# Kernel tuning notes

Measured on AMD Instinct MI355X. Metric: run time of the kernel, lower is better.

Reference implementation:

```python
import jax, jax.numpy as jnp
import numpy as np

N = 20000      # tuple-graph nodes
E = 320000     # edges per relation
F_IN = 5189    # 80 one-hot + 3*1703 node features
DIM = 256
N_ORIG = 183   # original texas graph nodes
C = 7


def _gcn(x, W, b, src, dst, n):
    # PyG GCNConv: add self loops, symmetric deg^-1/2 normalization, aggregate src->dst.
    loop = jnp.arange(n)
    s = jnp.concatenate([src, loop])
    d = jnp.concatenate([dst, loop])
    deg = jax.ops.segment_sum(jnp.ones(s.shape[0], x.dtype), d, num_segments=n)
    dinv = jnp.where(deg > 0, jax.lax.rsqrt(deg), 0.0)
    norm = dinv[s] * dinv[d]            # [E+n]
    h = x @ W                            # [n, dim]
    out = jax.ops.segment_sum(h[s] * norm[:, None], d, num_segments=n)
    return out + b


def _mlp(h, w1, b1, w2, b2):
    return jnp.maximum(h @ w1 + b1, 0.0) @ w2 + b2


def _seg_mean(h, idx, n):
    s = jax.ops.segment_sum(h, idx, num_segments=n)
    cnt = jax.ops.segment_sum(jnp.ones(idx.shape[0], h.dtype), idx, num_segments=n)
    return s / jnp.maximum(cnt, 1.0)[:, None]


def setup_inputs() -> dict:
    key = jax.random.key(0)
    ks = jax.random.split(key, 16)
    sc_in = 1.0 / np.sqrt(F_IN)
    sc_d = 1.0 / np.sqrt(DIM)
    sc_3d = 1.0 / np.sqrt(3 * DIM)
    inp = {
        'x': jax.random.normal(ks[0], (N, F_IN), jnp.float32),
        'w1': jax.random.normal(ks[1], (3, F_IN, DIM), jnp.float32) * sc_in,
        'b1': jnp.zeros((3, DIM), jnp.float32),
        'w2': jax.random.normal(ks[2], (3, DIM, DIM), jnp.float32) * sc_d,
        'b2': jnp.zeros((3, DIM), jnp.float32),
        'm1w1': jax.random.normal(ks[3], (3 * DIM, DIM), jnp.float32) * sc_3d,
        'm1b1': jnp.zeros((DIM,), jnp.float32),
        'm1w2': jax.random.normal(ks[4], (DIM, DIM), jnp.float32) * sc_d,
        'm1b2': jnp.zeros((DIM,), jnp.float32),
        'm2w1': jax.random.normal(ks[5], (3 * DIM, DIM), jnp.float32) * sc_3d,
        'm2b1': jnp.zeros((DIM,), jnp.float32),
        'm2w2': jax.random.normal(ks[6], (DIM, DIM), jnp.float32) * sc_d,
        'm2b2': jnp.zeros((DIM,), jnp.float32),
        'mw1': jax.random.normal(ks[7], (3 * DIM, DIM), jnp.float32) * sc_3d,
        'mb1': jnp.zeros((DIM,), jnp.float32),
        'mw2': jax.random.normal(ks[8], (DIM, C), jnp.float32) * sc_d,
        'mb2': jnp.zeros((C,), jnp.float32),
        'edge_index_1': jax.random.randint(ks[9], (2, E), 0, N),
        'edge_index_2': jax.random.randint(ks[10], (2, E), 0, N),
        'edge_index_3': jax.random.randint(ks[11], (2, E), 0, N),
        'index_1': jax.random.randint(ks[12], (N,), 0, N_ORIG),
        'index_2': jax.random.randint(ks[13], (N,), 0, N_ORIG),
        'index_3': jax.random.randint(ks[14], (N,), 0, N_ORIG),
    }
    return inp


def reference(x, w1, b1, w2, b2, m1w1, m1b1, m1w2, m1b2,
              m2w1, m2b1, m2w2, m2b2, mw1, mb1, mw2, mb2,
              edge_index_1, edge_index_2, edge_index_3,
              index_1, index_2, index_3):
    n = x.shape[0]
    eis = (edge_index_1, edge_index_2, edge_index_3)
    # layer 1: three GCN convs over the three relations, ReLU, concat, MLP
    hs = [jnp.maximum(_gcn(x, w1[i], b1[i], eis[i][0], eis[i][1], n), 0.0) for i in range(3)]
    h = _mlp(jnp.concatenate(hs, axis=-1), m1w1, m1b1, m1w2, m1b2)
    # layer 2
    hs = [jnp.maximum(_gcn(h, w2[i], b2[i], eis[i][0], eis[i][1], n), 0.0) for i in range(3)]
    h = _mlp(jnp.concatenate(hs, axis=-1), m2w1, m2b1, m2w2, m2b2)
    # faithful to source bug: index_2 is overwritten by index_3 before scatter
    x1 = _seg_mean(h, index_1, N_ORIG)
    x2 = _seg_mean(h, index_3, N_ORIG)
    x3 = _seg_mean(h, index_3, N_ORIG)
    out = _mlp(jnp.concatenate([x1, x2, x3], axis=1), mw1, mb1, mw2, mb2)
    return jax.nn.log_softmax(out, axis=1)
```

## Files before the change

kernel.cpp:

```cpp
#include <hip/hip_runtime.h>
#include <hip/hip_bf16.h>
#include <cstdint>
#include <cstddef>

typedef __bf16 bf16_t;
typedef __bf16 bf16x8 __attribute__((ext_vector_type(8)));
typedef __bf16 bf16x4 __attribute__((ext_vector_type(4)));
typedef float f32x4 __attribute__((ext_vector_type(4)));

#define NN 20000
#define NE 320000
#define FIN 5189
#define KP1 5216
#define NORIG 183

__device__ inline f32x4 ld4u(const float* p) {
  f32x4 v; __builtin_memcpy(&v, p, 16); return v;
}

__device__ inline void gload_lds16(const bf16_t* g, bf16_t* l) {
  __builtin_amdgcn_global_load_lds(
      (const __attribute__((address_space(1))) uint32_t*)g,
      (__attribute__((address_space(3))) uint32_t*)l, 16, 0, 0);
}

__device__ inline int swz(int r) { return (r ^ (r >> 2)) & 3; }

__global__ void k_cvtpad(const float* __restrict__ x, bf16_t* __restrict__ xb) {
  const int total = NN * (KP1 / 8);
  for (int idx = blockIdx.x * 256 + threadIdx.x; idx < total; idx += gridDim.x * 256) {
    int row = idx / (KP1 / 8);
    int c8  = idx - row * (KP1 / 8);
    int col = c8 * 8;
    bf16x8 v{};
    const float* xp = x + (size_t)row * FIN + col;
    if (col + 8 <= FIN) {
      f32x4 a = ld4u(xp), b = ld4u(xp + 4);
#pragma unroll
      for (int j = 0; j < 4; ++j) { v[j] = (bf16_t)a[j]; v[4 + j] = (bf16_t)b[j]; }
    } else {
#pragma unroll
      for (int j = 0; j < 8; ++j) v[j] = (col + j < FIN) ? (bf16_t)xp[j] : (bf16_t)0.f;
    }
    *(bf16x8*)&xb[(size_t)row * KP1 + col] = v;
  }
}

__global__ __launch_bounds__(512) void k_gemm_w(
    const bf16_t* __restrict__ A, const bf16_t* __restrict__ Bt,
    bf16_t* __restrict__ C, const float* __restrict__ bias,
    int M, int N, int Kp, int relu, int NBX)
{
  __shared__ __align__(16) bf16_t As[2][128 * 32];
  __shared__ __align__(16) bf16_t Bs[2][256 * 32];
  const int nwg = gridDim.x;
  const int q = nwg >> 3, rr = nwg & 7;
  const int xcd = blockIdx.x & 7, jj = blockIdx.x >> 3;
  const int L = (xcd < rr ? xcd * (q + 1) : rr * (q + 1) + (xcd - rr) * q) + jj;
  const int bx = L % NBX, by = L / NBX;

  const int tid = threadIdx.x, lane = tid & 63, wave = tid >> 6;
  const int m0 = by * 128, n0 = bx * 256;
  const int wr = (wave >> 2) * 64, wc = (wave & 3) * 64;
  const int fm = lane & 15, fs = lane >> 4;

  const int arow = tid >> 2, asl = tid & 3;
  const int aks = asl ^ swz(arow);
  int agrow = m0 + arow; if (agrow >= M) agrow = M - 1;
  const bf16_t* asrc = A + (size_t)agrow * Kp + aks * 8;

  const int br0 = tid >> 2, br1 = 128 + br0;
  const bf16_t* bsrc0 = Bt + (size_t)(n0 + br0) * Kp + (asl ^ swz(br0)) * 8;
  const bf16_t* bsrc1 = Bt + (size_t)(n0 + br1) * Kp + (asl ^ swz(br1)) * 8;

  bf16_t* adst  = &As[0][0] + wave * 512;
  bf16_t* bdst0 = &Bs[0][0] + wave * 512;
  bf16_t* bdst1 = &Bs[0][0] + 4096 + wave * 512;

  int aoff[4], boff[4];
#pragma unroll
  for (int i = 0; i < 4; ++i) {
    int ra = wr + i * 16 + fm;
    aoff[i] = ra * 32 + (fs ^ swz(ra)) * 8;
    int rb = wc + i * 16 + fm;
    boff[i] = rb * 32 + (fs ^ swz(rb)) * 8;
  }

  f32x4 acc[4][4];
#pragma unroll
  for (int i = 0; i < 4; ++i)
#pragma unroll
    for (int j = 0; j < 4; ++j) acc[i][j] = {0.f, 0.f, 0.f, 0.f};

#define STAGEW(buf, kof) do { \
    gload_lds16(asrc + (kof),  adst  + (buf) * (128 * 32)); \
    gload_lds16(bsrc0 + (kof), bdst0 + (buf) * (256 * 32)); \
    gload_lds16(bsrc1 + (kof), bdst1 + (buf) * (256 * 32)); \
  } while (0)

  const int NT = Kp / 32;
  STAGEW(0, 0);
  __syncthreads();
  int buf = 0;
  for (int t = 0; t < NT - 1; ++t) {
    STAGEW(buf ^ 1, (t + 1) * 32);
    bf16x8 af[4], bfv[4];
#pragma unroll
    for (int i = 0; i < 4; ++i) af[i] = *(const bf16x8*)&As[buf][aoff[i]];
#pragma unroll
    for (int j = 0; j < 4; ++j) bfv[j] = *(const bf16x8*)&Bs[buf][boff[j]];
#pragma unroll
    for (int i = 0; i < 4; ++i)
#pragma unroll
      for (int j = 0; j < 4; ++j)
        acc[i][j] = __builtin_amdgcn_mfma_f32_16x16x32_bf16(af[i], bfv[j], acc[i][j], 0, 0, 0);
    __syncthreads();
    buf ^= 1;
  }
  {
    bf16x8 af[4], bfv[4];
#pragma unroll
    for (int i = 0; i < 4; ++i) af[i] = *(const bf16x8*)&As[buf][aoff[i]];
#pragma unroll
    for (int j = 0; j < 4; ++j) bfv[j] = *(const bf16x8*)&Bs[buf][boff[j]];
#pragma unroll
    for (int i = 0; i < 4; ++i)
#pragma unroll
      for (int j = 0; j < 4; ++j)
        acc[i][j] = __builtin_amdgcn_mfma_f32_16x16x32_bf16(af[i], bfv[j], acc[i][j], 0, 0, 0);
  }

  const int ccol = n0 + wc + fm;
#pragma unroll
  for (int i = 0; i < 4; ++i) {
    const int rb2 = m0 + wr + i * 16 + (lane >> 4) * 4;
#pragma unroll
    for (int r = 0; r < 4; ++r) {
      const int row = rb2 + r;
      if (row < M) {
        bf16_t* cp = C + (size_t)row * N + ccol;
#pragma unroll
        for (int j = 0; j < 4; ++j) {
          float v = acc[i][j][r];
          if (bias) v += bias[ccol + j * 16];
          if (relu) v = fmaxf(v, 0.f);
          cp[j * 16] = (bf16_t)v;
        }
      }
    }
  }
}

__global__ __launch_bounds__(256) void k_gemm_s(
    const bf16_t* __restrict__ A, const bf16_t* __restrict__ Bt,
    bf16_t* __restrict__ C, const float* __restrict__ bias,
    int M, int N, int Kp, int relu)
{
  __shared__ __align__(16) bf16_t As[2][128 * 32];
  __shared__ __align__(16) bf16_t Bs[2][128 * 32];
  const int tid = threadIdx.x, lane = tid & 63, wave = tid >> 6;
  const int m0 = blockIdx.y * 128, n0 = blockIdx.x * 128;
  const int wr = (wave >> 1) * 64, wc = (wave & 1) * 64;
  const int fm = lane & 15, fs = lane >> 4;

  const int r0 = tid >> 2, r1 = 64 + r0, sl = tid & 3;
  int ag0 = m0 + r0; if (ag0 >= M) ag0 = M - 1;
  int ag1 = m0 + r1; if (ag1 >= M) ag1 = M - 1;
  const bf16_t* asrc0 = A + (size_t)ag0 * Kp + (sl ^ swz(r0)) * 8;
  const bf16_t* asrc1 = A + (size_t)ag1 * Kp + (sl ^ swz(r1)) * 8;
  const bf16_t* bsrc0 = Bt + (size_t)(n0 + r0) * Kp + (sl ^ swz(r0)) * 8;
  const bf16_t* bsrc1 = Bt + (size_t)(n0 + r1) * Kp + (sl ^ swz(r1)) * 8;

  bf16_t* adst0 = &As[0][0] + wave * 512;
  bf16_t* adst1 = &As[0][0] + 2048 + wave * 512;
  bf16_t* bdst0 = &Bs[0][0] + wave * 512;
  bf16_t* bdst1 = &Bs[0][0] + 2048 + wave * 512;

  int aoff[4], boff[4];
#pragma unroll
  for (int i = 0; i < 4; ++i) {
    int ra = wr + i * 16 + fm;
    aoff[i] = ra * 32 + (fs ^ swz(ra)) * 8;
    int rb = wc + i * 16 + fm;
    boff[i] = rb * 32 + (fs ^ swz(rb)) * 8;
  }

  f32x4 acc[4][4];
#pragma unroll
  for (int i = 0; i < 4; ++i)
#pragma unroll
    for (int j = 0; j < 4; ++j) acc[i][j] = {0.f, 0.f, 0.f, 0.f};

#define STAGES(buf, kof) do { \
    gload_lds16(asrc0 + (kof), adst0 + (buf) * (128 * 32)); \
    gload_lds16(asrc1 + (kof), adst1 + (buf) * (128 * 32)); \
    gload_lds16(bsrc0 + (kof), bdst0 + (buf) * (128 * 32)); \
    gload_lds16(bsrc1 + (kof), bdst1 + (buf) * (128 * 32)); \
  } while (0)

  const int NT = Kp / 32;
  STAGES(0, 0);
  __syncthreads();
  int buf = 0;
  for (int t = 0; t < NT - 1; ++t) {
    STAGES(buf ^ 1, (t + 1) * 32);
    bf16x8 af[4], bfv[4];
#pragma unroll
    for (int i = 0; i < 4; ++i) af[i] = *(const bf16x8*)&As[buf][aoff[i]];
#pragma unroll
    for (int j = 0; j < 4; ++j) bfv[j] = *(const bf16x8*)&Bs[buf][boff[j]];
#pragma unroll
    for (int i = 0; i < 4; ++i)
#pragma unroll
      for (int j = 0; j < 4; ++j)
        acc[i][j] = __builtin_amdgcn_mfma_f32_16x16x32_bf16(af[i], bfv[j], acc[i][j], 0, 0, 0);
    __syncthreads();
    buf ^= 1;
  }
  {
    bf16x8 af[4], bfv[4];
#pragma unroll
    for (int i = 0; i < 4; ++i) af[i] = *(const bf16x8*)&As[buf][aoff[i]];
#pragma unroll
    for (int j = 0; j < 4; ++j) bfv[j] = *(const bf16x8*)&Bs[buf][boff[j]];
#pragma unroll
    for (int i = 0; i < 4; ++i)
#pragma unroll
      for (int j = 0; j < 4; ++j)
        acc[i][j] = __builtin_amdgcn_mfma_f32_16x16x32_bf16(af[i], bfv[j], acc[i][j], 0, 0, 0);
  }

  const int ccol = n0 + wc + fm;
#pragma unroll
  for (int i = 0; i < 4; ++i) {
    const int rb2 = m0 + wr + i * 16 + (lane >> 4) * 4;
#pragma unroll
    for (int r = 0; r < 4; ++r) {
      const int row = rb2 + r;
      if (row < M) {
        bf16_t* cp = C + (size_t)row * N + ccol;
#pragma unroll
        for (int j = 0; j < 4; ++j) {
          float v = acc[i][j][r];
          if (bias) v += bias[ccol + j * 16];
          if (relu) v = fmaxf(v, 0.f);
          cp[j * 16] = (bf16_t)v;
        }
      }
    }
  }
}

__global__ void k_transw(const float* __restrict__ src, bf16_t* __restrict__ dst,
                         int K, int Kp)
{
  __shared__ float tile[32][33];
  const int g = blockIdx.z;
  const int k0 = blockIdx.x * 32, j0 = blockIdx.y * 32;
  const int tx = threadIdx.x, ty = threadIdx.y;
  const float* sp = src + (size_t)g * K * 256;
#pragma unroll
  for (int i = 0; i < 4; ++i) {
    int k = k0 + ty + i * 8;
    tile[ty + i * 8][tx] = (k < K) ? sp[(size_t)k * 256 + j0 + tx] : 0.f;
  }
  __syncthreads();
  bf16_t* dp = dst + (size_t)g * 256 * Kp;
#pragma unroll
  for (int i = 0; i < 4; ++i) {
    int n = j0 + ty + i * 8;
    dp[(size_t)n * Kp + k0 + tx] = (bf16_t)tile[tx][ty + i * 8];
  }
}

__global__ void k_deg3(const int* __restrict__ e1, const int* __restrict__ e2,
                       const int* __restrict__ e3, int* __restrict__ deg) {
  int i = blockIdx.x * 256 + threadIdx.x;
  if (i >= 3 * NE) return;
  int r = i / NE, e = i - r * NE;
  const int* d = (r == 0 ? e1 : (r == 1 ? e2 : e3)) + NE;
  atomicAdd(&deg[r * NN + d[e]], 1);
}

__global__ void k_degi(const int* __restrict__ i1, const int* __restrict__ i3,
                       int* __restrict__ deg183) {
  int i = blockIdx.x * 256 + threadIdx.x;
  if (i >= 2 * NN) return;
  int r = i / NN, v = i - r * NN;
  int g = (r ? i3 : i1)[v];
  atomicAdd(&deg183[r * NORIG + g], 1);
}

__global__ void k_dinv(const int* __restrict__ deg, float* __restrict__ dinv) {
  int v = blockIdx.x * 256 + threadIdx.x;
  if (v < 3 * NN) dinv[v] = rsqrtf((float)(deg[v] + 1));
}

#define SCAN_T 1024
#define SCAN_CH 20
__global__ __launch_bounds__(SCAN_T) void k_scan(
    const int* __restrict__ deg, int* __restrict__ rp, int* __restrict__ cur)
{
  const int r = blockIdx.x;
  const int* d = deg + r * NN;
  int* rpr = rp + r * (NN + 1);
  int* cr  = cur + r * NN;
  __shared__ int ts[SCAN_T];
  const int t = threadIdx.x;
  const int base = t * SCAN_CH;
  int local[SCAN_CH];
  int sum = 0;
#pragma unroll
  for (int i = 0; i < SCAN_CH; ++i) {
    int v = base + i;
    int x = (v < NN) ? d[v] : 0;
    local[i] = sum; sum += x;
  }
  ts[t] = sum; __syncthreads();
  for (int ofs = 1; ofs < SCAN_T; ofs <<= 1) {
    int v = ts[t];
    int w = (t >= ofs) ? ts[t - ofs] : 0;
    __syncthreads();
    ts[t] = v + w;
    __syncthreads();
  }
  int excl = (t == 0) ? 0 : ts[t - 1];
#pragma unroll
  for (int i = 0; i < SCAN_CH; ++i) {
    int v = base + i;
    if (v < NN) { int val = excl + local[i]; rpr[v] = val; cr[v] = val; }
  }
  if (t == SCAN_T - 1) rpr[NN] = ts[SCAN_T - 1];
}

__global__ void k_scan183(const int* __restrict__ deg183, int* __restrict__ rpg,
                          int* __restrict__ cur183) {
  const int r = blockIdx.x;
  const int* d = deg183 + r * NORIG;
  int* rpr = rpg + r * (NORIG + 1);
  int* cr  = cur183 + r * NORIG;
  __shared__ int ts[256];
  const int t = threadIdx.x;
  int x = (t < NORIG) ? d[t] : 0;
  ts[t] = x; __syncthreads();
  for (int o = 1; o < 256; o <<= 1) {
    int v = ts[t];
    int w = (t >= o) ? ts[t - o] : 0;
    __syncthreads();
    ts[t] = v + w;
    __syncthreads();
  }
  if (t < NORIG) {
    int excl = ts[t] - x;
    rpr[t] = excl; cr[t] = excl;
    if (t == NORIG - 1) rpr[NORIG] = ts[t];
  }
}

__global__ void k_bucket3(const int* __restrict__ e1, const int* __restrict__ e2,
                          const int* __restrict__ e3, int* __restrict__ cur,
                          int* __restrict__ col) {
  int i = blockIdx.x * 256 + threadIdx.x;
  if (i >= 3 * NE) return;
  int r = i / NE, e = i - r * NE;
  const int* ei = (r == 0 ? e1 : (r == 1 ? e2 : e3));
  int d = ei[NE + e];
  int pos = atomicAdd(&cur[r * NN + d], 1);
  col[(size_t)r * NE + pos] = ei[e];
}

__global__ void k_bucketi(const int* __restrict__ i1, const int* __restrict__ i3,
                          int* __restrict__ cur183, int* __restrict__ colg) {
  int i = blockIdx.x * 256 + threadIdx.x;
  if (i >= 2 * NN) return;
  int r = i / NN, v = i - r * NN;
  int g = (r ? i3 : i1)[v];
  int pos = atomicAdd(&cur183[r * NORIG + g], 1);
  colg[r * NN + pos] = v;
}

__global__ __launch_bounds__(256) void k_gatherb(
    const bf16_t* __restrict__ H, bf16_t* __restrict__ Out,
    const int* __restrict__ rp, const int* __restrict__ col,
    const float* __restrict__ dinv, const float* __restrict__ bias)
{
  const int wv = threadIdx.x >> 6, lane = threadIdx.x & 63;
  const int v = blockIdx.x * 4 + wv;
  const int r = blockIdx.y;
  const int roff = r << 8;
  const int* rpr = rp + r * (NN + 1);
  const int* cr  = col + (size_t)r * NE;
  const float* dvp = dinv + r * NN;
  const float dv = dvp[v];
  const int c0 = roff + lane * 4;

  bf16x4 hs = *(const bf16x4*)&H[(size_t)v * 768 + c0];
  float a0 = (float)hs[0] * dv, a1 = (float)hs[1] * dv,
        a2 = (float)hs[2] * dv, a3 = (float)hs[3] * dv;

  int i = rpr[v];
  const int e = rpr[v + 1];
  for (; i + 4 <= e; i += 4) {
    int s0 = cr[i], s1 = cr[i + 1], s2 = cr[i + 2], s3 = cr[i + 3];
    float d0 = dvp[s0], d1 = dvp[s1], d2 = dvp[s2], d3 = dvp[s3];
    bf16x4 h0 = *(const bf16x4*)&H[(size_t)s0 * 768 + c0];
    bf16x4 h1 = *(const bf16x4*)&H[(size_t)s1 * 768 + c0];
    bf16x4 h2 = *(const bf16x4*)&H[(size_t)s2 * 768 + c0];
    bf16x4 h3 = *(const bf16x4*)&H[(size_t)s3 * 768 + c0];
    a0 += (float)h0[0] * d0 + (float)h1[0] * d1 + (float)h2[0] * d2 + (float)h3[0] * d3;
    a1 += (float)h0[1] * d0 + (float)h1[1] * d1 + (float)h2[1] * d2 + (float)h3[1] * d3;
    a2 += (float)h0[2] * d0 + (float)h1[2] * d1 + (float)h2[2] * d2 + (float)h3[2] * d3;
    a3 += (float)h0[3] * d0 + (float)h1[3] * d1 + (float)h2[3] * d2 + (float)h3[3] * d3;
  }
  for (; i < e; ++i) {
    int s = cr[i];
    float d = dvp[s];
    bf16x4 h = *(const bf16x4*)&H[(size_t)s * 768 + c0];
    a0 += (float)h[0] * d; a1 += (float)h[1] * d;
    a2 += (float)h[2] * d; a3 += (float)h[3] * d;
  }
  f32x4 bb = ld4u(bias + c0);
  bf16x4 o;
  o[0] = (bf16_t)fmaxf(dv * a0 + bb[0], 0.f);
  o[1] = (bf16_t)fmaxf(dv * a1 + bb[1], 0.f);
  o[2] = (bf16_t)fmaxf(dv * a2 + bb[2], 0.f);
  o[3] = (bf16_t)fmaxf(dv * a3 + bb[3], 0.f);
  *(bf16x4*)&Out[(size_t)v * 768 + c0] = o;
}

__global__ __launch_bounds__(256) void k_final2(
    const bf16_t* __restrict__ h2,
    const int* __restrict__ rpg, const int* __restrict__ colg,
    const float* __restrict__ mw1, const float* __restrict__ mb1,
    const float* __restrict__ mw2, const float* __restrict__ mb2,
    float* __restrict__ out)
{
  __shared__ float xc[768];
  __shared__ float tt[256];
  __shared__ float lg[8];
  const int g = blockIdx.x, tid = threadIdx.x;
  const int* rp1 = rpg;
  const int* rp3 = rpg + (NORIG + 1);
  const int* c1v = colg;
  const int* c3v = colg + NN;

  float a1 = 0.f;
  int b1 = rp1[g], e1 = rp1[g + 1];
  for (int i = b1; i < e1; ++i) a1 += (float)h2[(size_t)c1v[i] * 256 + tid];
  float a3 = 0.f;
  int b3 = rp3[g], e3 = rp3[g + 1];
  for (int i = b3; i < e3; ++i) a3 += (float)h2[(size_t)c3v[i] * 256 + tid];
  a1 *= 1.f / fmaxf((float)(e1 - b1), 1.f);
  a3 *= 1.f / fmaxf((float)(e3 - b3), 1.f);
  xc[tid] = a1;
  xc[256 + tid] = a3;
  xc[512 + tid] = a3;
  __syncthreads();
  float acc = mb1[tid];
  for (int k = 0; k < 768; ++k) acc += xc[k] * mw1[k * 256 + tid];
  tt[tid] = fmaxf(acc, 0.f);
  __syncthreads();
  if (tid < 7) {
    float a = mb2[tid];
    for (int k = 0; k < 256; ++k) a += tt[k] * mw2[k * 7 + tid];
    lg[tid] = a;
  }
  __syncthreads();
  if (tid == 0) {
    float mx = lg[0];
    for (int c2 = 1; c2 < 7; ++c2) mx = fmaxf(mx, lg[c2]);
    float sum = 0.f;
    for (int c2 = 0; c2 < 7; ++c2) sum += expf(lg[c2] - mx);
    float lse = logf(sum) + mx;
    for (int c2 = 0; c2 < 7; ++c2) out[g * 7 + c2] = lg[c2] - lse;
  }
}

extern "C" void kernel_launch(void* const* d_in, const int* in_sizes, int n_in,
                              void* d_out, int out_size, void* d_ws, size_t ws_size,
                              hipStream_t stream) {
  const float* x    = (const float*)d_in[0];
  const float* w1   = (const float*)d_in[1];
  const float* b1   = (const float*)d_in[2];
  const float* w2   = (const float*)d_in[3];
  const float* b2   = (const float*)d_in[4];
  const float* m1w1 = (const float*)d_in[5];
  const float* m1b1 = (const float*)d_in[6];
  const float* m1w2 = (const float*)d_in[7];
  const float* m1b2 = (const float*)d_in[8];
  const float* m2w1 = (const float*)d_in[9];
  const float* m2b1 = (const float*)d_in[10];
  const float* m2w2 = (const float*)d_in[11];
  const float* m2b2 = (const float*)d_in[12];
  const float* mw1  = (const float*)d_in[13];
  const float* mb1  = (const float*)d_in[14];
  const float* mw2  = (const float*)d_in[15];
  const float* mb2  = (const float*)d_in[16];
  const int* e1 = (const int*)d_in[17];
  const int* e2 = (const int*)d_in[18];
  const int* e3 = (const int*)d_in[19];
  const int* i1 = (const int*)d_in[20];
  const int* i3 = (const int*)d_in[22];
  float* out = (float*)d_out;

  char* ws = (char*)d_ws;
  size_t off = 0;
  auto alloc = [&](size_t bytes) {
    char* p = ws + off;
    off += (bytes + 255) & ~(size_t)255;
    return (void*)p;
  };
  bf16_t* xb   = (bf16_t*)alloc((size_t)NN * KP1 * 2);
  bf16_t* wt   = (bf16_t*)alloc((size_t)768 * KP1 * 2);
  bf16_t* a1   = (bf16_t*)alloc((size_t)NN * 768 * 2);
  bf16_t* g1   = (bf16_t*)alloc((size_t)NN * 768 * 2);
  bf16_t* t1   = (bf16_t*)alloc((size_t)NN * 256 * 2);
  bf16_t* h1   = (bf16_t*)alloc((size_t)NN * 256 * 2);
  int*    deg  = (int*)alloc(((size_t)3 * NN + 2 * NORIG) * 4);
  float*  dinv = (float*)alloc((size_t)3 * NN * 4);
  int*    rp   = (int*)alloc((size_t)3 * (NN + 1) * 4);
  int*    cur  = (int*)alloc((size_t)3 * NN * 4);
  int*    col  = (int*)alloc((size_t)3 * NE * 4);
  int*    rpg  = (int*)alloc((size_t)2 * (NORIG + 1) * 4);
  int*    cur183 = (int*)alloc((size_t)2 * NORIG * 4);
  int*    colg = (int*)alloc((size_t)2 * NN * 4);
  int*    deg183 = deg + 3 * NN;

  hipMemsetAsync(deg, 0, ((size_t)3 * NN + 2 * NORIG) * 4, stream);
  k_deg3<<<(3 * NE + 255) / 256, 256, 0, stream>>>(e1, e2, e3, deg);
  k_degi<<<(2 * NN + 255) / 256, 256, 0, stream>>>(i1, i3, deg183);
  k_dinv<<<(3 * NN + 255) / 256, 256, 0, stream>>>(deg, dinv);
  k_scan<<<3, SCAN_T, 0, stream>>>(deg, rp, cur);
  k_scan183<<<2, 256, 0, stream>>>(deg183, rpg, cur183);
  k_bucket3<<<(3 * NE + 255) / 256, 256, 0, stream>>>(e1, e2, e3, cur, col);
  k_bucketi<<<(2 * NN + 255) / 256, 256, 0, stream>>>(i1, i3, cur183, colg);

  auto transw = [&](const float* Wsrc, int G, int K, int Kp) {
    k_transw<<<dim3(Kp / 32, 8, G), dim3(32, 8), 0, stream>>>(Wsrc, wt, K, Kp);
  };

  dim3 ggat(NN / 4, 3);
  const int NWG = 3 * 157;

  transw(w1, 3, FIN, KP1);
  k_cvtpad<<<2048, 256, 0, stream>>>(x, xb);
  k_gemm_w<<<NWG, 512, 0, stream>>>(xb, wt, a1, nullptr, NN, 768, KP1, 0, 3);
  k_gatherb<<<ggat, 256, 0, stream>>>(a1, g1, rp, col, dinv, b1);
  transw(m1w1, 1, 768, 768);
  k_gemm_s<<<dim3(2, 157), 256, 0, stream>>>(g1, wt, t1, m1b1, NN, 256, 768, 1);
  transw(m1w2, 1, 256, 256);
  k_gemm_s<<<dim3(2, 157), 256, 0, stream>>>(t1, wt, h1, m1b2, NN, 256, 256, 0);

  transw(w2, 3, 256, 256);
  k_gemm_w<<<NWG, 512, 0, stream>>>(h1, wt, a1, nullptr, NN, 768, 256, 0, 3);
  k_gatherb<<<ggat, 256, 0, stream>>>(a1, g1, rp, col, dinv, b2);
  transw(m2w1, 1, 768, 768);
  k_gemm_s<<<dim3(2, 157), 256, 0, stream>>>(g1, wt, t1, m2b1, NN, 256, 768, 1);
  transw(m2w2, 1, 256, 256);
  k_gemm_s<<<dim3(2, 157), 256, 0, stream>>>(t1, wt, h1, m2b2, NN, 256, 256, 0);

  k_final2<<<NORIG, 256, 0, stream>>>(h1, rpg, colg, mw1, mb1, mw2, mb2, out);
}
```

Measured before the change: 872.0 us.

## Add 256x256-tile GEMM with K=64 stages and interleaved loads for layer-1 projection

Adds a new bf16 MFMA GEMM kernel that uses 256x256 output tiles with a K step of 64, XOR-swizzled LDS layout, and global-to-LDS loads for the next stage split across four compute phases with priority hints. It replaces the 128x256 kernel only for the large K=5189 layer-1 projection, and KP1 is padded to a multiple of 64. The goal is more operand reuse per LDS load and better overlap of memory traffic with MFMA work. The trade-off is higher register and LDS pressure, only 237 workgroups, and a partly empty last M tile.

```diff
diff --git a/kernel.cpp b/kernel.cpp
--- a/kernel.cpp
+++ b/kernel.cpp
@@ -11,7 +11,7 @@
 #define NN 20000
 #define NE 320000
 #define FIN 5189
-#define KP1 5216
+#define KP1 5248
 #define NORIG 183
 
 __device__ inline f32x4 ld4u(const float* p) {
@@ -43,6 +43,159 @@
       for (int j = 0; j < 8; ++j) v[j] = (col + j < FIN) ? (bf16_t)xp[j] : (bf16_t)0.f;
     }
     *(bf16x8*)&xb[(size_t)row * KP1 + col] = v;
+  }
+}
+
+#define TOFF (256 * 64)
+
+__global__ __launch_bounds__(512, 2) void k_gemm8p(
+    const bf16_t* __restrict__ A, const bf16_t* __restrict__ Bt,
+    bf16_t* __restrict__ C, const float* __restrict__ bias,
+    int M, int N, int Kp, int relu, int NBX)
+{
+  __shared__ __align__(16) bf16_t As[2][TOFF];
+  __shared__ __align__(16) bf16_t Bs[2][TOFF];
+  const int nwg = gridDim.x;
+  const int q = nwg >> 3, rr = nwg & 7;
+  const int xcd = blockIdx.x & 7, jj = blockIdx.x >> 3;
+  const int L = (xcd < rr ? xcd * (q + 1) : rr * (q + 1) + (xcd - rr) * q) + jj;
+  const int bx = L % NBX, by = L / NBX;
+
+  const int tid = threadIdx.x, lane = tid & 63, wave = tid >> 6;
+  const int m0 = by * 256, n0 = bx * 256;
+  const int wr = (wave >> 2) * 128, wc = (wave & 3) * 64;
+  const int fm = lane & 15, fs = lane >> 4;
+
+  const int lrow = lane >> 3;
+  const int lcolc = ((lane & 7) ^ lrow) * 8;
+
+  int arow[4], brow[4];
+#pragma unroll
+  for (int c = 0; c < 4; ++c) {
+    int ro = wave * 16 + ((c & 1) * 8) + ((c >> 1) * 128) + lrow;
+    int ar = m0 + ro; if (ar >= M) ar = M - 1;
+    arow[c] = ar;
+    brow[c] = n0 + ro;
+  }
+  const bf16_t* ap0 = A + (size_t)arow[0] * Kp + lcolc;
+  const bf16_t* ap1 = A + (size_t)arow[1] * Kp + lcolc;
+  const bf16_t* ap2 = A + (size_t)arow[2] * Kp + lcolc;
+  const bf16_t* ap3 = A + (size_t)arow[3] * Kp + lcolc;
+  const bf16_t* bp0 = Bt + (size_t)brow[0] * Kp + lcolc;
+  const bf16_t* bp1 = Bt + (size_t)brow[1] * Kp + lcolc;
+  const bf16_t* bp2 = Bt + (size_t)brow[2] * Kp + lcolc;
+  const bf16_t* bp3 = Bt + (size_t)brow[3] * Kp + lcolc;
+  const int dA0 = (wave * 16) * 64,       dA1 = (wave * 16 + 8) * 64;
+  const int dA2 = (128 + wave * 16) * 64, dA3 = (128 + wave * 16 + 8) * 64;
+
+  int slx[2];
+#pragma unroll
+  for (int ks = 0; ks < 2; ++ks) slx[ks] = (((ks * 4 + fs) ^ (fm & 7)) * 8);
+  int aof[8], bof[4];
+#pragma unroll
+  for (int i = 0; i < 8; ++i) aof[i] = (wr + i * 16 + fm) * 64;
+#pragma unroll
+  for (int j = 0; j < 4; ++j) bof[j] = (wc + j * 16 + fm) * 64;
+
+  f32x4 acc[8][4];
+#pragma unroll
+  for (int i = 0; i < 8; ++i)
+#pragma unroll
+    for (int j = 0; j < 4; ++j) acc[i][j] = {0.f, 0.f, 0.f, 0.f};
+
+#define STG_A0(u_) do { int b_=(u_)&1; size_t ko=(size_t)(u_)*64; \
+    gload_lds16(ap0+ko, &As[b_][dA0]); gload_lds16(ap1+ko, &As[b_][dA1]); } while (0)
+#define STG_A1(u_) do { int b_=(u_)&1; size_t ko=(size_t)(u_)*64; \
+    gload_lds16(ap2+ko, &As[b_][dA2]); gload_lds16(ap3+ko, &As[b_][dA3]); } while (0)
+#define STG_B0(u_) do { int b_=(u_)&1; size_t ko=(size_t)(u_)*64; \
+    gload_lds16(bp0+ko, &Bs[b_][dA0]); gload_lds16(bp1+ko, &Bs[b_][dA1]); } while (0)
+#define STG_B1(u_) do { int b_=(u_)&1; size_t ko=(size_t)(u_)*64; \
+    gload_lds16(bp2+ko, &Bs[b_][dA2]); gload_lds16(bp3+ko, &Bs[b_][dA3]); } while (0)
+
+#define PHASE(mh, ks, STGX) do { \
+    STGX; \
+    bf16x8 b0v = *(const bf16x8*)&Bs[b][bof[0] + slx[ks]]; \
+    bf16x8 b1v = *(const bf16x8*)&Bs[b][bof[1] + slx[ks]]; \
+    bf16x8 b2v = *(const bf16x8*)&Bs[b][bof[2] + slx[ks]]; \
+    bf16x8 b3v = *(const bf16x8*)&Bs[b][bof[3] + slx[ks]]; \
+    bf16x8 a0v = *(const bf16x8*)&As[b][aof[(mh)*4+0] + slx[ks]]; \
+    bf16x8 a1v = *(const bf16x8*)&As[b][aof[(mh)*4+1] + slx[ks]]; \
+    bf16x8 a2v = *(const bf16x8*)&As[b][aof[(mh)*4+2] + slx[ks]]; \
+    bf16x8 a3v = *(const bf16x8*)&As[b][aof[(mh)*4+3] + slx[ks]]; \
+    __builtin_amdgcn_s_setprio(1); \
+    acc[(mh)*4+0][0] = __builtin_amdgcn_mfma_f32_16x16x32_bf16(a0v, b0v, acc[(mh)*4+0][0], 0,0,0); \
+    acc[(mh)*4+0][1] = __builtin_amdgcn_mfma_f32_16x16x32_bf16(a0v, b1v, acc[(mh)*4+0][1], 0,0,0); \
+    acc[(mh)*4+0][2] = __builtin_amdgcn_mfma_f32_16x16x32_bf16(a0v, b2v, acc[(mh)*4+0][2], 0,0,0); \
+    acc[(mh)*4+0][3] = __builtin_amdgcn_mfma_f32_16x16x32_bf16(a0v, b3v, acc[(mh)*4+0][3], 0,0,0); \
+    acc[(mh)*4+1][0] = __builtin_amdgcn_mfma_f32_16x16x32_bf16(a1v, b0v, acc[(mh)*4+1][0], 0,0,0); \
+    acc[(mh)*4+1][1] = __builtin_amdgcn_mfma_f32_16x16x32_bf16(a1v, b1v, acc[(mh)*4+1][1], 0,0,0); \
+    acc[(mh)*4+1][2] = __builtin_amdgcn_mfma_f32_16x16x32_bf16(a1v, b2v, acc[(mh)*4+1][2], 0,0,0); \
+    acc[(mh)*4+1][3] = __builtin_amdgcn_mfma_f32_16x16x32_bf16(a1v, b3v, acc[(mh)*4+1][3], 0,0,0); \
+    acc[(mh)*4+2][0] = __builtin_amdgcn_mfma_f32_16x16x32_bf16(a2v, b0v, acc[(mh)*4+2][0], 0,0,0); \
+    acc[(mh)*4+2][1] = __builtin_amdgcn_mfma_f32_16x16x32_bf16(a2v, b1v, acc[(mh)*4+2][1], 0,0,0); \
+    acc[(mh)*4+2][2] = __builtin_amdgcn_mfma_f32_16x16x32_bf16(a2v, b2v, acc[(mh)*4+2][2], 0,0,0); \
+    acc[(mh)*4+2][3] = __builtin_amdgcn_mfma_f32_16x16x32_bf16(a2v, b3v, acc[(mh)*4+2][3], 0,0,0); \
+    acc[(mh)*4+3][0] = __builtin_amdgcn_mfma_f32_16x16x32_bf16(a3v, b0v, acc[(mh)*4+3][0], 0,0,0); \
+    acc[(mh)*4+3][1] = __builtin_amdgcn_mfma_f32_16x16x32_bf16(a3v, b1v, acc[(mh)*4+3][1], 0,0,0); \
+    acc[(mh)*4+3][2] = __builtin_amdgcn_mfma_f32_16x16x32_bf16(a3v, b2v, acc[(mh)*4+3][2], 0,0,0); \
+    acc[(mh)*4+3][3] = __builtin_amdgcn_mfma_f32_16x16x32_bf16(a3v, b3v, acc[(mh)*4+3][3], 0,0,0); \
+    __builtin_amdgcn_s_setprio(0); \
+  } while (0)
+
+  const int NT = Kp / 64;
+  STG_A0(0); STG_A1(0); STG_B0(0); STG_B1(0);
+
+  for (int u = 0; u < NT; ++u) {
+    const int b = u & 1;
+    __builtin_amdgcn_sched_barrier(0);
+    __builtin_amdgcn_s_barrier();
+    __builtin_amdgcn_sched_barrier(0);
+    if (u + 1 < NT) {
+      STG_A0(u + 1);
+      asm volatile("s_waitcnt vmcnt(2)" ::: "memory");
+    } else {
+      asm volatile("s_waitcnt vmcnt(0)" ::: "memory");
+    }
+    __builtin_amdgcn_sched_barrier(0);
+    __builtin_amdgcn_s_barrier();
+    __builtin_amdgcn_sched_barrier(0);
+
+    if (u + 1 < NT) {
+      PHASE(0, 0, );
+      PHASE(1, 0, STG_A1(u + 1));
+      PHASE(0, 1, STG_B0(u + 1));
+      PHASE(1, 1, STG_B1(u + 1));
+    } else {
+      PHASE(0, 0, );
+      PHASE(1, 0, );
+      PHASE(0, 1, );
+      PHASE(1, 1, );
+    }
+  }
+#undef PHASE
+#undef STG_A0
+#undef STG_A1
+#undef STG_B0
+#undef STG_B1
+
+  const int ccol = n0 + wc + fm;
+#pragma unroll
+  for (int i = 0; i < 8; ++i) {
+    const int rb2 = m0 + wr + i * 16 + (lane >> 4) * 4;
+#pragma unroll
+    for (int r = 0; r < 4; ++r) {
+      const int row = rb2 + r;
+      if (row < M) {
+        bf16_t* cp = C + (size_t)row * N + ccol;
+#pragma unroll
+        for (int j = 0; j < 4; ++j) {
+          float v = acc[i][j][r];
+          if (bias) v += bias[ccol + j * 16];
+          if (relu) v = fmaxf(v, 0.f);
+          cp[j * 16] = (bf16_t)v;
+        }
+      }
+    }
   }
 }
 
@@ -540,11 +693,12 @@
   };
 
   dim3 ggat(NN / 4, 3);
-  const int NWG = 3 * 157;
+  const int NWG8 = 3 * 79;
+  const int NWGW = 3 * 157;
 
   transw(w1, 3, FIN, KP1);
   k_cvtpad<<<2048, 256, 0, stream>>>(x, xb);
-  k_gemm_w<<<NWG, 512, 0, stream>>>(xb, wt, a1, nullptr, NN, 768, KP1, 0, 3);
+  k_gemm8p<<<NWG8, 512, 0, stream>>>(xb, wt, a1, nullptr, NN, 768, KP1, 0, 3);
   k_gatherb<<<ggat, 256, 0, stream>>>(a1, g1, rp, col, dinv, b1);
   transw(m1w1, 1, 768, 768);
   k_gemm_s<<<dim3(2, 157), 256, 0, stream>>>(g1, wt, t1, m1b1, NN, 256, 768, 1);
@@ -552,7 +706,7 @@
   k_gemm_s<<<dim3(2, 157), 256, 0, stream>>>(t1, wt, h1, m1b2, NN, 256, 256, 0);
 
   transw(w2, 3, 256, 256);
-  k_gemm_w<<<NWG, 512, 0, stream>>>(h1, wt, a1, nullptr, NN, 768, 256, 0, 3);
+  k_gemm_w<<<NWGW, 512, 0, stream>>>(h1, wt, a1, nullptr, NN, 768, 256, 0, 3);
   k_gatherb<<<ggat, 256, 0, stream>>>(a1, g1, rp, col, dinv, b2);
   transw(m2w1, 1, 768, 768);
   k_gemm_s<<<dim3(2, 157), 256, 0, stream>>>(g1, wt, t1, m2b1, NN, 256, 768, 1);
```

After: 2.355 ms. 2.7x slower.
